# Kernel tuning notes

Hardware: AMD Instinct MI355X
Metric: run time of the kernel (lower is better)

Reference implementation:

```python
import jax, jax.numpy as jnp
import numpy as np


def _lstm_scan(x_proj, Wr, units):
    """x_proj: [T, B, 4U] precomputed x@Wk + b. Keras gate order: i, f, g(c), o.
    Returns (all_h [T,B,U], last_h [B,U])."""
    B = x_proj.shape[1]
    h0 = jnp.zeros((B, units), x_proj.dtype)
    c0 = jnp.zeros((B, units), x_proj.dtype)

    def step(carry, xt):
        h, c = carry
        z = xt + h @ Wr                      # [B, 4U]
        i, f, g, o = jnp.split(z, 4, axis=-1)
        i = jax.nn.sigmoid(i)
        f = jax.nn.sigmoid(f)
        g = jnp.tanh(g)
        o = jax.nn.sigmoid(o)
        c = f * c + i * g
        h = o * jnp.tanh(c)
        return (h, c), h

    (h_T, _), hs = jax.lax.scan(step, (h0, c0), x_proj)
    return hs, h_T


def bilstm(x, Wk_f, Wr_f, b_f, Wk_b, Wr_b, b_b):
    units = Wr_f.shape[0]
    # Precompute input projections for all timesteps (one big GEMM per direction)
    xp_f = (x @ Wk_f + b_f).transpose(1, 0, 2)             # [T, B, 4U]
    xp_b = (x[:, ::-1] @ Wk_b + b_b).transpose(1, 0, 2)    # reversed time

    fw_hs, fw_last = _lstm_scan(xp_f, Wr_f, units)         # [T,B,U], [B,U]
    bw_hs, bw_last = _lstm_scan(xp_b, Wr_b, units)

    fw_outputs = fw_hs.transpose(1, 0, 2)                  # [B, T, U]
    # go_backwards outputs are in reverse time order; K.reverse(_, 1) re-aligns
    bw_outputs = bw_hs.transpose(1, 0, 2)[:, ::-1]         # [B, T, U]

    outputs = jnp.concatenate([fw_outputs, bw_outputs], axis=-1)   # [B, T, 2U]
    last_output = jnp.concatenate([fw_last, bw_last], axis=-1)     # [B, 2U]
    return outputs, last_output


def setup_inputs() -> dict:
    key = jax.random.key(0)
    ks = jax.random.split(key, 6)
    B, T, D, U = 32, 512, 256, 256
    s_in = 1.0 / np.sqrt(D)
    s_rec = 1.0 / np.sqrt(U)
    return {
        "x": jax.random.normal(ks[0], (B, T, D), jnp.float32),
        "Wk_f": jax.random.normal(ks[1], (D, 4 * U), jnp.float32) * s_in,
        "Wr_f": jax.random.normal(ks[2], (U, 4 * U), jnp.float32) * s_rec,
        "b_f": jnp.zeros((4 * U,), jnp.float32),
        "Wk_b": jax.random.normal(ks[3], (D, 4 * U), jnp.float32) * s_in,
        "Wr_b": jax.random.normal(ks[4], (U, 4 * U), jnp.float32) * s_rec,
        "b_b": jnp.zeros((4 * U,), jnp.float32),
    }


def reference(x, Wk_f, Wr_f, b_f, Wk_b, Wr_b, b_b):
    return bilstm(x, Wk_f, Wr_f, b_f, Wk_b, Wr_b, b_b)
```

## Files before the change

### kernel.cpp

```cpp
#include <hip/hip_runtime.h>

#define T_STEPS 512
#define BATCH   32
#define DIM     256
#define UNITS   256
#define COLS4U  1024

typedef _Float16 half8 __attribute__((ext_vector_type(8)));
typedef float    f32x4 __attribute__((ext_vector_type(4)));
typedef float    f32x4n __attribute__((ext_vector_type(4)));
typedef unsigned long long ull;
typedef ull      ull2  __attribute__((ext_vector_type(2)));

__device__ __forceinline__ float fsig(float x){ return 1.0f/(1.0f+__expf(-x)); }
__device__ __forceinline__ float ftanh(float x){
  float xx = fminf(fmaxf(x,-15.f),15.f);
  float e = __expf(2.f*xx);
  return (e-1.f)/(e+1.f);
}

__device__ __forceinline__ int swz(int b, int u){
  int g = u >> 3;
  int s = (g & 7) ^ (b & 7);
  return b*512 + (g>>3)*128 + s*16 + (u & 7)*2;
}

__global__ __launch_bounds__(256,1) void bilstm_mfma(
    const float* __restrict__ x,
    const float* __restrict__ Wk_f, const float* __restrict__ Wr_f, const float* __restrict__ b_f,
    const float* __restrict__ Wk_b, const float* __restrict__ Wr_b, const float* __restrict__ b_b,
    float* __restrict__ out,
    unsigned short* __restrict__ slices,
    unsigned* __restrict__ flags)
{
  const int dir = blockIdx.x >> 2;
  const int g4  = blockIdx.x & 3;
  const int tid = threadIdx.x;
  const int w   = tid >> 6;
  const int lane= tid & 63;
  const int l15 = lane & 15;
  const int l4  = lane >> 4;

  const float* Wk = dir ? Wk_b : Wk_f;
  const float* Wr = dir ? Wr_b : Wr_f;
  const float* bs = dir ? b_b  : b_f;

  const int u0b   = g4*64;
  const int upl   = u0b + w*16 + l15;
  const int outcol= dir*256 + upl;

  __shared__ _Float16 xlds[BATCH*DIM];
  __shared__ _Float16 hlds[2][BATCH*UNITS];

  half8 Bf[4][16];
#pragma unroll
  for (int q=0;q<4;q++){
    const int col = q*256 + upl;
#pragma unroll
    for (int kk=0;kk<16;kk++){
      const float* Ws = (kk<8) ? Wk : Wr;
      const int k0 = (kk&7)*32 + l4*8;
      half8 v;
#pragma unroll
      for (int r=0;r<8;r++) v[r] = (_Float16)Ws[(size_t)(k0+r)*COLS4U + col];
      Bf[q][kk] = v;
      __builtin_amdgcn_sched_barrier(0);
    }
  }

  float bias[4];
#pragma unroll
  for (int q=0;q<4;q++) bias[q] = bs[q*256 + upl];

  {
    half8 z;
#pragma unroll
    for (int e=0;e<8;e++) z[e] = (_Float16)0.f;
    for (int i=tid; i<BATCH*UNITS/8; i+=256) ((half8*)hlds[0])[i] = z;
  }

  const int bx  = tid >> 3;
  const int d0x = (tid & 7) * 32;
  float xr[32];
  {
    const int tin0 = dir ? (T_STEPS-1) : 0;
    const float* xp = x + ((size_t)bx*T_STEPS + tin0)*DIM + d0x;
#pragma unroll
    for (int i=0;i<8;i++){
      f32x4 v = *(const f32x4*)(xp + i*4);
      xr[i*4+0]=v[0]; xr[i*4+1]=v[1]; xr[i*4+2]=v[2]; xr[i*4+3]=v[3];
    }
#pragma unroll
    for (int j=0;j<4;j++){
      half8 hh;
#pragma unroll
      for (int e=0;e<8;e++) hh[e] = (_Float16)xr[j*8+e];
      *(half8*)((char*)xlds + swz(bx, d0x + j*8)) = hh;
    }
  }
  __syncthreads();

  float cst[8];
#pragma unroll
  for (int i=0;i<8;i++) cst[i]=0.f;
  bool spin_ok = true;

  for (int t=0; t<T_STEPS; ++t){
    if (t+1 < T_STEPS){
      const int tin = dir ? (T_STEPS-2-t) : (t+1);
      const float* xp = x + ((size_t)bx*T_STEPS + tin)*DIM + d0x;
#pragma unroll
      for (int i=0;i<8;i++){
        f32x4 v = *(const f32x4*)(xp + i*4);
        xr[i*4+0]=v[0]; xr[i*4+1]=v[1]; xr[i*4+2]=v[2]; xr[i*4+3]=v[3];
      }
    }

    f32x4 acc[2][4];
#pragma unroll
    for (int q=0;q<4;q++){
      f32x4 a; a[0]=bias[q]; a[1]=bias[q]; a[2]=bias[q]; a[3]=bias[q];
      acc[0][q]=a; acc[1][q]=a;
    }
    const char* hpl = (const char*)hlds[t&1];
#pragma unroll
    for (int kk=0;kk<16;kk++){
      const char* pl = (kk<8) ? (const char*)xlds : hpl;
      const int ul = (kk&7)*32 + l4*8;
      half8 a0 = *(const half8*)(pl + swz(l15,      ul));
      half8 a1 = *(const half8*)(pl + swz(16+l15,   ul));
#pragma unroll
      for (int q=0;q<4;q++){
        acc[0][q] = __builtin_amdgcn_mfma_f32_16x16x32_f16(a0, Bf[q][kk], acc[0][q], 0,0,0);
        acc[1][q] = __builtin_amdgcn_mfma_f32_16x16x32_f16(a1, Bf[q][kk], acc[1][q], 0,0,0);
      }
    }

    const int tout = dir ? (T_STEPS-1-t) : t;
    unsigned short* slc = slices + (((size_t)((t+1)&1))*8 + dir*4 + g4)*2048;
    char* hnx = (char*)hlds[(t+1)&1];
#pragma unroll
    for (int mt=0; mt<2; mt++){
#pragma unroll
      for (int r=0;r<4;r++){
        const int b = mt*16 + l4*4 + r;
        float iv = fsig (acc[mt][0][r]);
        float fv = fsig (acc[mt][1][r]);
        float gv = ftanh(acc[mt][2][r]);
        float ov = fsig (acc[mt][3][r]);
        float &c = cst[mt*4+r];
        c = fv*c + iv*gv;
        float hv = ov*ftanh(c);
        out[((size_t)b*T_STEPS + tout)*(2*UNITS) + outcol] = hv;
        if (t == T_STEPS-1)
          out[(size_t)BATCH*T_STEPS*(2*UNITS) + (size_t)b*(2*UNITS) + outcol] = hv;
        _Float16 hf = (_Float16)hv;
        *(_Float16*)(hnx + swz(b, upl)) = hf;
        if (t+1 < T_STEPS)
          __hip_atomic_store(&slc[b*64 + (w*16+l15)],
                             __builtin_bit_cast(unsigned short, hf),
                             __ATOMIC_RELAXED, __HIP_MEMORY_SCOPE_AGENT);
      }
    }
    __syncthreads();

    if (t+1 < T_STEPS){
      if (tid == 192)
        __hip_atomic_store(&flags[(dir*4+g4)*32], (unsigned)(t+1),
                           __ATOMIC_RELAXED, __HIP_MEMORY_SCOPE_AGENT);
#pragma unroll
      for (int j=0;j<4;j++){
        half8 hh;
#pragma unroll
        for (int e=0;e<8;e++) hh[e] = (_Float16)xr[j*8+e];
        *(half8*)((char*)xlds + swz(bx, d0x + j*8)) = hh;
      }
      if (w < 3){
        const int p = w + (w >= g4);
        const unsigned target = (unsigned)(t+1);
        if (spin_ok){
          int sp = 0;
          while (__hip_atomic_load(&flags[(dir*4+p)*32],
                                   __ATOMIC_RELAXED, __HIP_MEMORY_SCOPE_AGENT) < target){
            if (++sp > (1<<22)) { spin_ok = false; break; }
          }
        }
        const ull* src = (const ull*)(slices + (((size_t)((t+1)&1))*8 + dir*4 + p)*2048);
        const int bsl = lane >> 1;
        const int u00 = (lane & 1) * 32;
#pragma unroll
        for (int j=0;j<4;j++){
          ull v0 = __hip_atomic_load(&src[lane*8 + 2*j  ], __ATOMIC_RELAXED, __HIP_MEMORY_SCOPE_AGENT);
          ull v1 = __hip_atomic_load(&src[lane*8 + 2*j+1], __ATOMIC_RELAXED, __HIP_MEMORY_SCOPE_AGENT);
          ull2 vv; vv[0]=v0; vv[1]=v1;
          *(ull2*)(hnx + swz(bsl, p*64 + u00 + j*8)) = vv;
        }
      }
      __syncthreads();
    }
  }
}

extern "C" void kernel_launch(void* const* d_in, const int* in_sizes, int n_in,
                              void* d_out, int out_size, void* d_ws, size_t ws_size,
                              hipStream_t stream) {
  const float* x    = (const float*)d_in[0];
  const float* Wk_f = (const float*)d_in[1];
  const float* Wr_f = (const float*)d_in[2];
  const float* b_f  = (const float*)d_in[3];
  const float* Wk_b = (const float*)d_in[4];
  const float* Wr_b = (const float*)d_in[5];
  const float* b_b  = (const float*)d_in[6];
  float* out = (float*)d_out;

  unsigned short* slices = (unsigned short*)d_ws;
  unsigned* flags = (unsigned*)((char*)d_ws + 65536);

  hipMemsetAsync((char*)d_ws + 65536, 0, 1024, stream);

  bilstm_mfma<<<8, 256, 0, stream>>>(x, Wk_f, Wr_f, b_f, Wk_b, Wr_b, b_b,
                                     out, slices, flags);
}
```

Measured before the change: 2.399 ms.

## Precompute input projection in parallel kernel and halve recurrent scan block count

Moves the x@Wk input projection out of the sequential scan into a separate, massively parallel MFMA kernel that writes fp16 pre-activations to workspace. The recurrent scan then uses 4 blocks of 512 threads (two per direction) instead of 8 blocks, so each step does only the h@Wr product. Cross-block exchange moves from a separate flag to per-element step tags packed with the fp16 value, which cuts sync partners from three to one. The costs are a large workspace buffer, extra fp16 rounding of the projection, and a fallback path when the workspace is too small.

```diff
diff --git a/kernel.cpp b/kernel.cpp
--- a/kernel.cpp
+++ b/kernel.cpp
@@ -6,11 +6,11 @@
 #define UNITS   256
 #define COLS4U  1024
 
-typedef _Float16 half8 __attribute__((ext_vector_type(8)));
-typedef float    f32x4 __attribute__((ext_vector_type(4)));
-typedef float    f32x4n __attribute__((ext_vector_type(4)));
+typedef _Float16 half8  __attribute__((ext_vector_type(8)));
+typedef _Float16 half4v __attribute__((ext_vector_type(4)));
+typedef float    f32x4  __attribute__((ext_vector_type(4)));
 typedef unsigned long long ull;
-typedef ull      ull2  __attribute__((ext_vector_type(2)));
+typedef ull      ull2   __attribute__((ext_vector_type(2)));
 
 __device__ __forceinline__ float fsig(float x){ return 1.0f/(1.0f+__expf(-x)); }
 __device__ __forceinline__ float ftanh(float x){
@@ -23,6 +23,257 @@
   int g = u >> 3;
   int s = (g & 7) ^ (b & 7);
   return b*512 + (g>>3)*128 + s*16 + (u & 7)*2;
+}
+
+__global__ __launch_bounds__(256, 2) void xproj(
+    const float* __restrict__ x,
+    const float* __restrict__ Wk_f, const float* __restrict__ b_f,
+    const float* __restrict__ Wk_b, const float* __restrict__ b_b,
+    _Float16* __restrict__ xph)
+{
+  const int bx  = blockIdx.x;
+  const int dir = bx >> 8;
+  const int cg  = (bx >> 5) & 7;
+  const int tg  = bx & 31;
+  const int tid = threadIdx.x;
+  const int w   = tid >> 6;
+  const int lane= tid & 63;
+  const int l15 = lane & 15;
+  const int l4  = lane >> 4;
+
+  const float* Wk = dir ? Wk_b : Wk_f;
+  const float* bs = dir ? b_b  : b_f;
+
+  const int col0 = cg*128 + w*32;
+
+  half8 Bf[2][8];
+  float bias[2];
+#pragma unroll
+  for (int nt=0; nt<2; nt++){
+    const int col = col0 + nt*16 + l15;
+    bias[nt] = bs[col];
+#pragma unroll
+    for (int kk=0; kk<8; kk++){
+      half8 v;
+#pragma unroll
+      for (int r=0; r<8; r++) v[r] = (_Float16)Wk[(size_t)(kk*32 + l4*8 + r)*COLS4U + col];
+      Bf[nt][kk] = v;
+    }
+  }
+
+  for (int tt=0; tt<16; ++tt){
+    const int t   = tg*16 + tt;
+    const int tin = dir ? (T_STEPS-1-t) : t;
+
+    half8 Af[2][8];
+#pragma unroll
+    for (int mt=0; mt<2; mt++){
+      const int b = mt*16 + l15;
+#pragma unroll
+      for (int kk=0; kk<8; kk++){
+        const float* xp_ = x + ((size_t)b*T_STEPS + tin)*DIM + kk*32 + l4*8;
+        f32x4 u0 = *(const f32x4*)xp_;
+        f32x4 u1 = *(const f32x4*)(xp_ + 4);
+        half8 v;
+        v[0]=(_Float16)u0[0]; v[1]=(_Float16)u0[1]; v[2]=(_Float16)u0[2]; v[3]=(_Float16)u0[3];
+        v[4]=(_Float16)u1[0]; v[5]=(_Float16)u1[1]; v[6]=(_Float16)u1[2]; v[7]=(_Float16)u1[3];
+        Af[mt][kk] = v;
+      }
+    }
+
+    f32x4 acc[2][2];
+#pragma unroll
+    for (int nt=0; nt<2; nt++){
+      f32x4 a; a[0]=bias[nt]; a[1]=bias[nt]; a[2]=bias[nt]; a[3]=bias[nt];
+      acc[nt][0]=a; acc[nt][1]=a;
+    }
+#pragma unroll
+    for (int kk=0; kk<8; kk++)
+#pragma unroll
+      for (int nt=0; nt<2; nt++)
+#pragma unroll
+        for (int mt=0; mt<2; mt++)
+          acc[nt][mt] = __builtin_amdgcn_mfma_f32_16x16x32_f16(Af[mt][kk], Bf[nt][kk], acc[nt][mt], 0,0,0);
+
+#pragma unroll
+    for (int nt=0; nt<2; nt++){
+      const int col = col0 + nt*16 + l15;
+#pragma unroll
+      for (int mt=0; mt<2; mt++){
+        half4v o;
+        o[0]=(_Float16)acc[nt][mt][0]; o[1]=(_Float16)acc[nt][mt][1];
+        o[2]=(_Float16)acc[nt][mt][2]; o[3]=(_Float16)acc[nt][mt][3];
+        *(ull*)(xph + ((size_t)(dir*T_STEPS + t)*COLS4U + col)*BATCH + mt*16 + l4*4)
+            = __builtin_bit_cast(ull, o);
+      }
+    }
+  }
+}
+
+__global__ __launch_bounds__(512, 2) void bilstm_scan4(
+    const float* __restrict__ Wr_f, const float* __restrict__ Wr_b,
+    float* __restrict__ out,
+    const _Float16* __restrict__ xph,
+    unsigned* __restrict__ slices)
+{
+  const int dir  = blockIdx.x >> 1;
+  const int half = blockIdx.x & 1;
+  const int tid  = threadIdx.x;
+  const int w    = tid >> 6;
+  const int lane = tid & 63;
+  const int l15  = lane & 15;
+  const int l4   = lane >> 4;
+
+  const float* Wr = dir ? Wr_b : Wr_f;
+
+  const int uloc   = w*16 + l15;
+  const int unit   = half*128 + uloc;
+  const int outcol = dir*256 + unit;
+
+  __shared__ _Float16 hlds[2][BATCH*UNITS];
+
+  half8 Bf[4][8];
+#pragma unroll
+  for (int q=0; q<4; q++){
+    const int col = q*256 + unit;
+#pragma unroll
+    for (int kk=0; kk<8; kk++){
+      half8 v;
+#pragma unroll
+      for (int r=0; r<8; r++) v[r] = (_Float16)Wr[(size_t)(kk*32 + l4*8 + r)*COLS4U + col];
+      Bf[q][kk] = v;
+      __builtin_amdgcn_sched_barrier(0);
+    }
+  }
+
+  {
+    half8 z;
+#pragma unroll
+    for (int e=0; e<8; e++) z[e] = (_Float16)0.f;
+    for (int i=tid; i<BATCH*UNITS/8; i+=512) ((half8*)hlds[0])[i] = z;
+  }
+  __syncthreads();
+
+  const int b_r = tid >> 4;
+  const int c0  = (tid & 15) * 8;
+  const int pbase = (1-half)*128;
+
+  float cst[8];
+#pragma unroll
+  for (int i=0;i<8;i++) cst[i]=0.f;
+  bool spin_ok = true;
+
+  ull xpv[8];
+#pragma unroll
+  for (int q=0;q<4;q++)
+#pragma unroll
+    for (int mt=0;mt<2;mt++)
+      xpv[q*2+mt] = *(const ull*)(xph + ((size_t)(dir*T_STEPS + 0)*COLS4U + q*256+unit)*BATCH + mt*16 + l4*4);
+
+  for (int t=0; t<T_STEPS; ++t){
+    f32x4 acc[2][4];
+#pragma unroll
+    for (int q=0;q<4;q++)
+#pragma unroll
+      for (int mt=0;mt<2;mt++){
+        half4v hv = __builtin_bit_cast(half4v, xpv[q*2+mt]);
+        f32x4 a; a[0]=(float)hv[0]; a[1]=(float)hv[1]; a[2]=(float)hv[2]; a[3]=(float)hv[3];
+        acc[mt][q] = a;
+      }
+
+    const char* hpl = (const char*)hlds[t&1];
+#pragma unroll
+    for (int kk=0; kk<8; kk++){
+      const int ul = kk*32 + l4*8;
+      half8 a0 = *(const half8*)(hpl + swz(l15,    ul));
+      half8 a1 = *(const half8*)(hpl + swz(16+l15, ul));
+#pragma unroll
+      for (int q=0;q<4;q++){
+        acc[0][q] = __builtin_amdgcn_mfma_f32_16x16x32_f16(a0, Bf[q][kk], acc[0][q], 0,0,0);
+        acc[1][q] = __builtin_amdgcn_mfma_f32_16x16x32_f16(a1, Bf[q][kk], acc[1][q], 0,0,0);
+      }
+    }
+
+    const int tout = dir ? (T_STEPS-1-t) : t;
+    const int par  = (t+1) & 1;
+    unsigned* myslc = slices + ((size_t)(par*4 + dir*2 + half))*4096;
+    const unsigned tgt_out = (unsigned)(t+1) & 0xFFFFu;
+    char* hnx = (char*)hlds[(t+1)&1];
+#pragma unroll
+    for (int mt=0; mt<2; mt++){
+#pragma unroll
+      for (int r=0;r<4;r++){
+        const int b = mt*16 + l4*4 + r;
+        float iv = fsig (acc[mt][0][r]);
+        float fv = fsig (acc[mt][1][r]);
+        float gv = ftanh(acc[mt][2][r]);
+        float ov = fsig (acc[mt][3][r]);
+        float &c = cst[mt*4+r];
+        c = fv*c + iv*gv;
+        float hv = ov*ftanh(c);
+        _Float16 hf = (_Float16)hv;
+        if (t+1 < T_STEPS){
+          unsigned word = ((unsigned)__builtin_bit_cast(unsigned short, hf) << 16) | tgt_out;
+          __hip_atomic_store(&myslc[b*128 + uloc], word,
+                             __ATOMIC_RELAXED, __HIP_MEMORY_SCOPE_AGENT);
+        }
+        *(_Float16*)(hnx + swz(b, unit)) = hf;
+        out[((size_t)b*T_STEPS + tout)*(2*UNITS) + outcol] = hv;
+        if (t == T_STEPS-1)
+          out[(size_t)BATCH*T_STEPS*(2*UNITS) + (size_t)b*(2*UNITS) + outcol] = hv;
+      }
+    }
+
+    if (t+1 < T_STEPS){
+#pragma unroll
+      for (int q=0;q<4;q++)
+#pragma unroll
+        for (int mt=0;mt<2;mt++)
+          xpv[q*2+mt] = *(const ull*)(xph + ((size_t)(dir*T_STEPS + (t+1))*COLS4U + q*256+unit)*BATCH + mt*16 + l4*4);
+
+      const ull* src = (const ull*)(slices + ((size_t)(par*4 + dir*2 + (1-half)))*4096
+                                    + b_r*128 + c0);
+      ull v0,v1,v2,v3;
+      if (spin_ok){
+        int sp = 0; bool ok;
+        do {
+          v0 = __hip_atomic_load(&src[0], __ATOMIC_RELAXED, __HIP_MEMORY_SCOPE_AGENT);
+          v1 = __hip_atomic_load(&src[1], __ATOMIC_RELAXED, __HIP_MEMORY_SCOPE_AGENT);
+          v2 = __hip_atomic_load(&src[2], __ATOMIC_RELAXED, __HIP_MEMORY_SCOPE_AGENT);
+          v3 = __hip_atomic_load(&src[3], __ATOMIC_RELAXED, __HIP_MEMORY_SCOPE_AGENT);
+          unsigned t0=(unsigned)v0, t1=(unsigned)(v0>>32), t2=(unsigned)v1, t3=(unsigned)(v1>>32);
+          unsigned t4=(unsigned)v2, t5=(unsigned)(v2>>32), t6=(unsigned)v3, t7=(unsigned)(v3>>32);
+          ok = ((t0&0xFFFF)==tgt_out) & ((t1&0xFFFF)==tgt_out) & ((t2&0xFFFF)==tgt_out)
+             & ((t3&0xFFFF)==tgt_out) & ((t4&0xFFFF)==tgt_out) & ((t5&0xFFFF)==tgt_out)
+             & ((t6&0xFFFF)==tgt_out) & ((t7&0xFFFF)==tgt_out);
+          if (++sp > (1<<20)) { spin_ok = false; break; }
+        } while(!ok);
+      } else {
+        v0 = __hip_atomic_load(&src[0], __ATOMIC_RELAXED, __HIP_MEMORY_SCOPE_AGENT);
+        v1 = __hip_atomic_load(&src[1], __ATOMIC_RELAXED, __HIP_MEMORY_SCOPE_AGENT);
+        v2 = __hip_atomic_load(&src[2], __ATOMIC_RELAXED, __HIP_MEMORY_SCOPE_AGENT);
+        v3 = __hip_atomic_load(&src[3], __ATOMIC_RELAXED, __HIP_MEMORY_SCOPE_AGENT);
+      }
+      half8 hv;
+      {
+        unsigned wlo, whi;
+        wlo=(unsigned)v0; whi=(unsigned)(v0>>32);
+        hv[0]=__builtin_bit_cast(_Float16,(unsigned short)(wlo>>16));
+        hv[1]=__builtin_bit_cast(_Float16,(unsigned short)(whi>>16));
+        wlo=(unsigned)v1; whi=(unsigned)(v1>>32);
+        hv[2]=__builtin_bit_cast(_Float16,(unsigned short)(wlo>>16));
+        hv[3]=__builtin_bit_cast(_Float16,(unsigned short)(whi>>16));
+        wlo=(unsigned)v2; whi=(unsigned)(v2>>32);
+        hv[4]=__builtin_bit_cast(_Float16,(unsigned short)(wlo>>16));
+        hv[5]=__builtin_bit_cast(_Float16,(unsigned short)(whi>>16));
+        wlo=(unsigned)v3; whi=(unsigned)(v3>>32);
+        hv[6]=__builtin_bit_cast(_Float16,(unsigned short)(wlo>>16));
+        hv[7]=__builtin_bit_cast(_Float16,(unsigned short)(whi>>16));
+      }
+      *(half8*)(hnx + swz(b_r, pbase + c0)) = hv;
+    }
+    __syncthreads();
+  }
 }
 
 __global__ __launch_bounds__(256,1) void bilstm_mfma(
@@ -150,11 +401,11 @@
         float ov = fsig (acc[mt][3][r]);
         float &c = cst[mt*4+r];
         c = fv*c + iv*gv;
-        float hv = ov*ftanh(c);
-        out[((size_t)b*T_STEPS + tout)*(2*UNITS) + outcol] = hv;
+        float hval = ov*ftanh(c);
+        out[((size_t)b*T_STEPS + tout)*(2*UNITS) + outcol] = hval;
         if (t == T_STEPS-1)
-          out[(size_t)BATCH*T_STEPS*(2*UNITS) + (size_t)b*(2*UNITS) + outcol] = hv;
-        _Float16 hf = (_Float16)hv;
+          out[(size_t)BATCH*T_STEPS*(2*UNITS) + (size_t)b*(2*UNITS) + outcol] = hval;
+        _Float16 hf = (_Float16)hval;
         *(_Float16*)(hnx + swz(b, upl)) = hf;
         if (t+1 < T_STEPS)
           __hip_atomic_store(&slc[b*64 + (w*16+l15)],
@@ -213,11 +464,19 @@
   const float* b_b  = (const float*)d_in[6];
   float* out = (float*)d_out;
 
-  unsigned short* slices = (unsigned short*)d_ws;
-  unsigned* flags = (unsigned*)((char*)d_ws + 65536);
-
-  hipMemsetAsync((char*)d_ws + 65536, 0, 1024, stream);
-
-  bilstm_mfma<<<8, 256, 0, stream>>>(x, Wk_f, Wr_f, b_f, Wk_b, Wr_b, b_b,
-                                     out, slices, flags);
-}
+  const size_t XPH = (size_t)2*T_STEPS*COLS4U*BATCH*sizeof(_Float16);
+  const size_t SL  = (size_t)2*2*2*BATCH*128*sizeof(unsigned);
+
+  if (ws_size >= XPH + SL) {
+    _Float16* xph    = (_Float16*)d_ws;
+    unsigned* slices = (unsigned*)((char*)d_ws + XPH);
+    xproj<<<512, 256, 0, stream>>>(x, Wk_f, b_f, Wk_b, b_b, xph);
+    bilstm_scan4<<<4, 512, 0, stream>>>(Wr_f, Wr_b, out, xph, slices);
+  } else {
+    unsigned short* slices = (unsigned short*)d_ws;
+    unsigned* flags = (unsigned*)((char*)d_ws + 65536);
+    hipMemsetAsync((char*)d_ws + 65536, 0, 1024, stream);
+    bilstm_mfma<<<8, 256, 0, stream>>>(x, Wk_f, Wr_f, b_f, Wk_b, Wr_b, b_b,
+                                       out, slices, flags);
+  }
+}
```

Measured after the change: 2.842 ms. 1.18x slower.
